# Kernel optimization log

Hardware: AMD Instinct MI355X
Metric: run time of the kernel (lower is better)

The kernel has to match this reference:

```python
import jax, jax.numpy as jnp
import numpy as np

B, T, H, NH, V = 2, 2048, 512, 8, 32000
HD = H // NH  # head dim

def setup_inputs() -> dict:
    key = jax.random.key(0)
    ks = jax.random.split(key, 15)
    s = 0.02
    rn = lambda k, shp: (jax.random.normal(k, shp, dtype=jnp.float32) * s)
    return {
        "ixs": jax.random.randint(ks[0], (B, T), 0, V, dtype=jnp.int32),
        "tok_emb": rn(ks[1], (V, H)),
        "pos_emb": rn(ks[2], (1, T, H)),
        "W_prj": rn(ks[3], (H, H)),
        "Wq": rn(ks[4], (H, H)), "bq": rn(ks[5], (H,)),
        "Wk": rn(ks[6], (H, H)), "bk": rn(ks[7], (H,)),
        "Wv": rn(ks[8], (H, H)), "bv": rn(ks[9], (H,)),
        "W1": rn(ks[10], (H, H)), "b1": rn(ks[11], (H,)),
        "W2": rn(ks[12], (V, H)), "b2": rn(ks[13], (V,)),
    }

def reference(ixs, tok_emb, pos_emb, W_prj, Wq, bq, Wk, bk, Wv, bv, W1, b1, W2, b2):
    b, t = ixs.shape
    # embeddings + projection (prj1 has no bias)
    x = tok_emb[ixs] + pos_emb[:, :t, :]          # [B,T,H]
    x = x @ W_prj.T                                # [B,T,H]
    # multi-head causal attention; NOTE: scale uses full hidden dim (allH**0.5)
    def heads(W, bias):
        return (x @ W.T + bias).reshape(b, t, NH, HD).transpose(0, 2, 1, 3)  # [B,nH,T,HD]
    q, k, v = heads(Wq, bq), heads(Wk, bk), heads(Wv, bv)
    att = jnp.einsum('bhqd,bhkd->bhqk', q, k) / (H ** 0.5)  # [B,nH,T,T]
    causal = jnp.tril(jnp.ones((t, t), dtype=bool))
    att = jnp.where(causal, att, -jnp.inf)
    w = jax.nn.softmax(att, axis=-1)
    y = jnp.einsum('bhqk,bhkd->bhqd', w, v)        # [B,nH,T,HD]
    y = y.transpose(0, 2, 1, 3).reshape(b, t, H)   # [B,T,H]
    # MLP: Linear->ReLU->Linear->ReLU (final ReLU per original loop condition)
    h1 = jax.nn.relu(y @ W1.T + b1)                # [B,T,H]
    out = jax.nn.relu(h1 @ W2.T + b2)              # [B,T,V]
    return out
```

## Files before the change

### kernel.cpp

```cpp
#include <hip/hip_runtime.h>
#include <stdint.h>
#include <stddef.h>

#define TSEQ   2048
#define HDIM   512
#define NHEADS 8
#define HEADD  64
#define NVOCAB 32000
#define NROWS  4096

typedef unsigned short ushort_t;
typedef __bf16 bf16x8 __attribute__((ext_vector_type(8)));
typedef float  f32x4  __attribute__((ext_vector_type(4)));
typedef unsigned short us8 __attribute__((ext_vector_type(8)));
typedef unsigned short us4 __attribute__((ext_vector_type(4)));
typedef unsigned short us2 __attribute__((ext_vector_type(2)));

__device__ __forceinline__ ushort_t f2bf(float f){
  union { float f; unsigned int u; } v; v.f = f;
  unsigned int u = v.u;
  u += 0x7FFFu + ((u >> 16) & 1u);
  return (ushort_t)(u >> 16);
}

__device__ __forceinline__ void gload_lds16(const ushort_t* g, ushort_t* l){
  __builtin_amdgcn_global_load_lds(
      (const __attribute__((address_space(1))) void*)g,
      (__attribute__((address_space(3))) void*)l, 16, 0, 0);
}

#define CVT_N4   4423680
#define CVT_TOT  4424064
__global__ void cvt_all_kernel(const float* __restrict__ Wprj, const float* __restrict__ Wq,
                               const float* __restrict__ Wk,   const float* __restrict__ Wv,
                               const float* __restrict__ W1,   const float* __restrict__ W2,
                               const float* __restrict__ bq,   const float* __restrict__ bk,
                               const float* __restrict__ bv,
                               ushort_t* __restrict__ wdst, float* __restrict__ bqkv){
  int stride = gridDim.x * blockDim.x;
  for (int i = blockIdx.x * blockDim.x + threadIdx.x; i < CVT_TOT; i += stride){
    if (i < CVT_N4){
      const float* src; int j;
      if (i < 327680){
        int w = i >> 16;
        j = i & 65535;
        src = (w == 0) ? Wprj : (w == 1) ? Wq : (w == 2) ? Wk : (w == 3) ? Wv : W1;
      } else {
        j = i - 327680;
        src = W2;
      }
      float4 f = ((const float4*)src)[j];
      us4 o;
      o[0] = f2bf(f.x); o[1] = f2bf(f.y); o[2] = f2bf(f.z); o[3] = f2bf(f.w);
      ((us4*)wdst)[i] = o;
    } else {
      int j = i - CVT_N4;
      const float* src = (j < 128) ? bq : (j < 256) ? bk : bv;
      int jj = j & 127;
      ((float4*)bqkv)[j] = ((const float4*)src)[jj];
    }
  }
}

__global__ void embed_kernel(const int* __restrict__ ixs, const float* __restrict__ tok,
                             const float* __restrict__ pos, ushort_t* __restrict__ x0){
  const int r = blockIdx.x;
  const int t = r & (TSEQ - 1);
  const int ix = ixs[r];
  const int j = threadIdx.x;
  const float2 a = ((const float2*)(tok + (size_t)ix * HDIM))[j];
  const float2 p = ((const float2*)(pos + (size_t)t * HDIM))[j];
  us2 o; o[0] = f2bf(a.x + p.x); o[1] = f2bf(a.y + p.y);
  *(us2*)(x0 + (size_t)r * HDIM + j * 2) = o;
}

template<int HAS_BIAS, int RELU, int OUT_F32>
__global__ __launch_bounds__(256) void gemm_bt_kernel(
    const ushort_t* __restrict__ A, const ushort_t* __restrict__ W,
    const float* __restrict__ bias, void* __restrict__ outp,
    int M, int N, int K)
{
  __shared__ ushort_t As[128 * 64];
  __shared__ ushort_t Bs[128 * 64];
  const int tid  = threadIdx.x;
  const int wave = tid >> 6;
  const int lane = tid & 63;
  const int lr   = lane & 15;
  const int lg   = lane >> 4;
  const int nby  = M >> 7;
  const int by   = blockIdx.x % nby;
  const int bx   = blockIdx.x / nby;
  const int row0 = by << 7;
  const int col0 = bx << 7;
  const int wr   = wave >> 1, wc = wave & 1;

  f32x4 acc[4][4];
#pragma unroll
  for (int m = 0; m < 4; m++)
#pragma unroll
    for (int n = 0; n < 4; n++) acc[m][n] = (f32x4){0.f, 0.f, 0.f, 0.f};

  const int e    = tid * 8;
  const int srow = e >> 6;
  const int scol = e & 63;
  const ushort_t* gA = A + (size_t)(row0 + srow) * K + scol;
  const ushort_t* gB = W + (size_t)(col0 + srow) * K + scol;
  const int ldsbase = wave * 512;

  for (int kt = 0; kt < K; kt += 64){
#pragma unroll
    for (int p = 0; p < 4; p++){
      gload_lds16(gA + (size_t)(p * 32) * K + kt, &As[p * 2048 + ldsbase]);
      gload_lds16(gB + (size_t)(p * 32) * K + kt, &Bs[p * 2048 + ldsbase]);
    }
    __syncthreads();
#pragma unroll
    for (int kk = 0; kk < 64; kk += 32){
      bf16x8 af[4], bfr[4];
#pragma unroll
      for (int m = 0; m < 4; m++)
        af[m] = __builtin_bit_cast(bf16x8,
            *(const us8*)&As[(wr * 64 + m * 16 + lr) * 64 + kk + lg * 8]);
#pragma unroll
      for (int n = 0; n < 4; n++)
        bfr[n] = __builtin_bit_cast(bf16x8,
            *(const us8*)&Bs[(wc * 64 + n * 16 + lr) * 64 + kk + lg * 8]);
#pragma unroll
      for (int m = 0; m < 4; m++)
#pragma unroll
        for (int n = 0; n < 4; n++)
          acc[m][n] = __builtin_amdgcn_mfma_f32_16x16x32_bf16(af[m], bfr[n], acc[m][n], 0, 0, 0);
    }
    __syncthreads();
  }

#pragma unroll
  for (int n = 0; n < 4; n++){
    const int col = col0 + wc * 64 + n * 16 + lr;
    float bv = 0.f;
    if (HAS_BIAS) bv = bias[col];
#pragma unroll
    for (int m = 0; m < 4; m++){
      const int rowb = row0 + wr * 64 + m * 16 + lg * 4;
#pragma unroll
      for (int r = 0; r < 4; r++){
        float vv = acc[m][n][r] + bv;
        if (RELU) vv = fmaxf(vv, 0.f);
        const size_t o = (size_t)(rowb + r) * N + col;
        if (OUT_F32) ((float*)outp)[o] = vv;
        else         ((ushort_t*)outp)[o] = f2bf(vv);
      }
    }
  }
}

__global__ __launch_bounds__(256) void attn_kernel(
    const ushort_t* __restrict__ qkv, ushort_t* __restrict__ y)
{
  __shared__ ushort_t Ks[64 * 64];
  __shared__ ushort_t Vt[64 * 64];
  __shared__ ushort_t Ps[4][16 * 64];
  const int qt   = blockIdx.x;
  const int hb   = blockIdx.y;
  const int b    = hb >> 3;
  const int h    = hb & 7;
  const int tid  = threadIdx.x;
  const int wave = tid >> 6, lane = tid & 63;
  const int lr   = lane & 15, lg = lane >> 4;
  const int ld   = 3 * HDIM;
  const size_t rowbase = (size_t)b * TSEQ;
  const ushort_t* kb = qkv + HDIM;
  const ushort_t* vb = qkv + 2 * HDIM;

  const int qrow = qt * 64 + wave * 16 + lr;
  const ushort_t* qp = qkv + (rowbase + qrow) * ld + h * HEADD;
  bf16x8 qf[2];
  qf[0] = __builtin_bit_cast(bf16x8, *(const us8*)&qp[lg * 8]);
  qf[1] = __builtin_bit_cast(bf16x8, *(const us8*)&qp[32 + lg * 8]);

  float m_run[4], l_run[4];
  f32x4 acc_o[4];
#pragma unroll
  for (int i = 0; i < 4; i++){ m_run[i] = -1e30f; l_run[i] = 0.f; acc_o[i] = (f32x4){0,0,0,0}; }

  const int e    = tid * 8;
  const int srow = e >> 6;
  const int scol = e & 63;
  const float scale = 0.04419417382415922f;

  for (int kt = 0; kt <= qt; ++kt){
    const ushort_t* gK = kb + (rowbase + kt * 64 + srow) * ld + h * HEADD + scol;
    gload_lds16(gK,                     &Ks[wave * 512]);
    gload_lds16(gK + (size_t)32 * ld,   &Ks[2048 + wave * 512]);
    const ushort_t* gV = vb + (rowbase + kt * 64 + srow) * ld + h * HEADD + scol;
    us8 v0 = *(const us8*)gV;
    us8 v1 = *(const us8*)(gV + (size_t)32 * ld);
#pragma unroll
    for (int j = 0; j < 8; j++){
      Vt[(scol + j) * 64 + srow]      = v0[j];
      Vt[(scol + j) * 64 + srow + 32] = v1[j];
    }
    __syncthreads();

    f32x4 s[4];
#pragma unroll
    for (int n = 0; n < 4; n++){
      s[n] = (f32x4){0, 0, 0, 0};
#pragma unroll
      for (int ks = 0; ks < 2; ks++){
        bf16x8 kf = __builtin_bit_cast(bf16x8,
            *(const us8*)&Ks[(n * 16 + lr) * 64 + ks * 32 + lg * 8]);
        s[n] = __builtin_amdgcn_mfma_f32_16x16x32_bf16(qf[ks], kf, s[n], 0, 0, 0);
      }
    }

    float sv[4][4];
    float tmax[4] = {-1e30f, -1e30f, -1e30f, -1e30f};
    const bool diag = (kt == qt);
#pragma unroll
    for (int n = 0; n < 4; n++)
#pragma unroll
      for (int r = 0; r < 4; r++){
        float x = s[n][r] * scale;
        if (diag && (n * 16 + lr) > (wave * 16 + lg * 4 + r)) x = -1e30f;
        sv[n][r] = x;
        tmax[r] = fmaxf(tmax[r], x);
      }
#pragma unroll
    for (int off = 1; off < 16; off <<= 1)
#pragma unroll
      for (int r = 0; r < 4; r++) tmax[r] = fmaxf(tmax[r], __shfl_xor(tmax[r], off));

    float alpha[4], psum[4];
#pragma unroll
    for (int r = 0; r < 4; r++){
      float mn = fmaxf(m_run[r], tmax[r]);
      alpha[r] = __expf(m_run[r] - mn);
      m_run[r] = mn;
      psum[r] = 0.f;
    }
    float p[4][4];
#pragma unroll
    for (int n = 0; n < 4; n++)
#pragma unroll
      for (int r = 0; r < 4; r++){ p[n][r] = __expf(sv[n][r] - m_run[r]); psum[r] += p[n][r]; }
#pragma unroll
    for (int off = 1; off < 16; off <<= 1)
#pragma unroll
      for (int r = 0; r < 4; r++) psum[r] += __shfl_xor(psum[r], off);
#pragma unroll
    for (int r = 0; r < 4; r++) l_run[r] = l_run[r] * alpha[r] + psum[r];
#pragma unroll
    for (int nd = 0; nd < 4; nd++)
#pragma unroll
      for (int r = 0; r < 4; r++) acc_o[nd][r] *= alpha[r];

#pragma unroll
    for (int n = 0; n < 4; n++)
#pragma unroll
      for (int r = 0; r < 4; r++)
        Ps[wave][(lg * 4 + r) * 64 + n * 16 + lr] = f2bf(p[n][r]);
    asm volatile("s_waitcnt lgkmcnt(0)" ::: "memory");
    bf16x8 pa[2];
    pa[0] = __builtin_bit_cast(bf16x8, *(const us8*)&Ps[wave][lr * 64 + lg * 8]);
    pa[1] = __builtin_bit_cast(bf16x8, *(const us8*)&Ps[wave][lr * 64 + 32 + lg * 8]);
#pragma unroll
    for (int nd = 0; nd < 4; nd++)
#pragma unroll
      for (int ks = 0; ks < 2; ks++){
        bf16x8 vf = __builtin_bit_cast(bf16x8,
            *(const us8*)&Vt[(nd * 16 + lr) * 64 + ks * 32 + lg * 8]);
        acc_o[nd] = __builtin_amdgcn_mfma_f32_16x16x32_bf16(pa[ks], vf, acc_o[nd], 0, 0, 0);
      }
    __syncthreads();
  }

  float inv[4];
#pragma unroll
  for (int r = 0; r < 4; r++) inv[r] = 1.f / l_run[r];
#pragma unroll
  for (int nd = 0; nd < 4; nd++)
#pragma unroll
    for (int r = 0; r < 4; r++){
      const int row_t = qt * 64 + wave * 16 + lg * 4 + r;
      y[(rowbase + row_t) * HDIM + h * HEADD + nd * 16 + lr] = f2bf(acc_o[nd][r] * inv[r]);
    }
}

extern "C" void kernel_launch(void* const* d_in, const int* in_sizes, int n_in,
                              void* d_out, int out_size, void* d_ws, size_t ws_size,
                              hipStream_t stream)
{
  const int*   ixs  = (const int*)  d_in[0];
  const float* tok  = (const float*)d_in[1];
  const float* pos  = (const float*)d_in[2];
  const float* Wprj = (const float*)d_in[3];
  const float* Wq   = (const float*)d_in[4];
  const float* bq_  = (const float*)d_in[5];
  const float* Wk   = (const float*)d_in[6];
  const float* bk_  = (const float*)d_in[7];
  const float* Wv   = (const float*)d_in[8];
  const float* bv_  = (const float*)d_in[9];
  const float* W1   = (const float*)d_in[10];
  const float* b1_  = (const float*)d_in[11];
  const float* W2   = (const float*)d_in[12];
  const float* b2_  = (const float*)d_in[13];
  float* out = (float*)d_out;

  ushort_t* ws    = (ushort_t*)d_ws;
  ushort_t* x0    = ws;
  ushort_t* x1    = x0    + 2097152;
  ushort_t* qkv   = x1    + 2097152;
  ushort_t* yb    = qkv   + 6291456;
  ushort_t* h1b   = yb    + 2097152;
  ushort_t* wprjb = h1b   + 2097152;
  ushort_t* wqkvb = wprjb + 262144;
  ushort_t* w1b   = wqkvb + 786432;
  ushort_t* w2b   = w1b   + 262144;
  float*    bqkv  = (float*)(w2b + 16384000);

  cvt_all_kernel<<<2048, 256, 0, stream>>>(Wprj, Wq, Wk, Wv, W1, W2,
                                           bq_, bk_, bv_, wprjb, bqkv);

  embed_kernel<<<NROWS, 256, 0, stream>>>(ixs, tok, pos, x0);

  gemm_bt_kernel<0,0,0><<<32 * 4,   256, 0, stream>>>(x0,  wprjb, nullptr, x1,  NROWS, 512,   512);
  gemm_bt_kernel<1,0,0><<<32 * 12,  256, 0, stream>>>(x1,  wqkvb, bqkv,    qkv, NROWS, 1536,  512);
  attn_kernel<<<dim3(32, 16), 256, 0, stream>>>(qkv, yb);
  gemm_bt_kernel<1,1,0><<<32 * 4,   256, 0, stream>>>(yb,  w1b,   b1_,     h1b, NROWS, 512,   512);
  gemm_bt_kernel<1,1,1><<<32 * 250, 256, 0, stream>>>(h1b, w2b,   b2_,     out, NROWS, NVOCAB, 512);
}
```

Baseline: 476.5 us.

## Add 256x256-tile triple-buffered GEMM kernel for vocab projection

```diff
diff --git a/kernel.cpp b/kernel.cpp
--- a/kernel.cpp
+++ b/kernel.cpp
@@ -154,6 +154,124 @@
   }
 }
 
+#define NKT 16
+__global__ __launch_bounds__(512, 2) void gemm_big_kernel(
+    const ushort_t* __restrict__ A, const ushort_t* __restrict__ W,
+    const float* __restrict__ bias, float* __restrict__ outp,
+    int M, int N, int K)
+{
+  __shared__ ushort_t Asb[3][256 * 32];
+  __shared__ ushort_t Bsb[3][256 * 32];
+  const int tid  = threadIdx.x;
+  const int wave = tid >> 6;
+  const int lane = tid & 63;
+  const int lr   = lane & 15;
+  const int lg   = lane >> 4;
+  const int wr   = wave >> 2;
+  const int wc   = wave & 3;
+  const int nby  = M >> 8;
+  const int by   = blockIdx.x % nby;
+  const int bx   = blockIdx.x / nby;
+  const int row0 = by << 8;
+  const int col0 = bx << 8;
+
+  const int rA   = tid >> 2;
+  const int csw  = ((tid & 3) ^ (rA & 3)) * 8;
+  const int swzc = (lg ^ (lr & 3)) * 8;
+
+  f32x4 acc[8][4];
+#pragma unroll
+  for (int m = 0; m < 8; m++)
+#pragma unroll
+    for (int n = 0; n < 4; n++) acc[m][n] = (f32x4){0.f, 0.f, 0.f, 0.f};
+
+  {
+    const ushort_t* gA = A + (size_t)(row0 + rA) * K + csw;
+    const ushort_t* gW = W + (size_t)(col0 + rA) * K + csw;
+#pragma unroll
+    for (int t = 0; t < 2; t++){
+      gload_lds16(gA + t * 32,                       &Asb[t][wave * 512]);
+      gload_lds16(gA + (size_t)128 * K + t * 32,     &Asb[t][4096 + wave * 512]);
+      gload_lds16(gW + t * 32,                       &Bsb[t][wave * 512]);
+      gload_lds16(gW + (size_t)128 * K + t * 32,     &Bsb[t][4096 + wave * 512]);
+    }
+  }
+  asm volatile("s_waitcnt vmcnt(4)" ::: "memory");
+  __builtin_amdgcn_s_barrier();
+
+  for (int t = 0; t < NKT; ++t){
+    const ushort_t* Ac = &Asb[t % 3][0];
+    const ushort_t* Bc = &Bsb[t % 3][0];
+    ushort_t* An = &Asb[(t + 2) % 3][0];
+    ushort_t* Bn = &Bsb[(t + 2) % 3][0];
+    const bool pf = (t + 2 < NKT);
+    const int kg = (t + 2) * 32;
+
+    bf16x8 bfr[4], af[4];
+#pragma unroll
+    for (int n = 0; n < 4; n++)
+      bfr[n] = __builtin_bit_cast(bf16x8,
+          *(const us8*)&Bc[(wc * 64 + n * 16 + lr) * 32 + swzc]);
+#pragma unroll
+    for (int q = 0; q < 4; q++)
+      af[q] = __builtin_bit_cast(bf16x8,
+          *(const us8*)&Ac[(wr * 128 + q * 16 + lr) * 32 + swzc]);
+    if (pf){
+      gload_lds16(A + (size_t)(row0 + rA) * K + kg + csw,       An + wave * 512);
+      gload_lds16(A + (size_t)(row0 + rA + 128) * K + kg + csw, An + 4096 + wave * 512);
+    }
+    __builtin_amdgcn_s_barrier();
+    asm volatile("s_waitcnt lgkmcnt(0)" ::: "memory");
+    __builtin_amdgcn_sched_barrier(0);
+    __builtin_amdgcn_s_setprio(1);
+#pragma unroll
+    for (int q = 0; q < 4; q++)
+#pragma unroll
+      for (int n = 0; n < 4; n++)
+        acc[q][n] = __builtin_amdgcn_mfma_f32_16x16x32_bf16(af[q], bfr[n], acc[q][n], 0, 0, 0);
+    __builtin_amdgcn_s_setprio(0);
+    __builtin_amdgcn_sched_barrier(0);
+    __builtin_amdgcn_s_barrier();
+
+#pragma unroll
+    for (int q = 0; q < 4; q++)
+      af[q] = __builtin_bit_cast(bf16x8,
+          *(const us8*)&Ac[(wr * 128 + (q + 4) * 16 + lr) * 32 + swzc]);
+    if (pf){
+      gload_lds16(W + (size_t)(col0 + rA) * K + kg + csw,       Bn + wave * 512);
+      gload_lds16(W + (size_t)(col0 + rA + 128) * K + kg + csw, Bn + 4096 + wave * 512);
+    }
+    __builtin_amdgcn_s_barrier();
+    asm volatile("s_waitcnt lgkmcnt(0)" ::: "memory");
+    __builtin_amdgcn_sched_barrier(0);
+    __builtin_amdgcn_s_setprio(1);
+#pragma unroll
+    for (int q = 0; q < 4; q++)
+#pragma unroll
+      for (int n = 0; n < 4; n++)
+        acc[q + 4][n] = __builtin_amdgcn_mfma_f32_16x16x32_bf16(af[q], bfr[n], acc[q + 4][n], 0, 0, 0);
+    __builtin_amdgcn_s_setprio(0);
+    __builtin_amdgcn_sched_barrier(0);
+    if (t < NKT - 2) { asm volatile("s_waitcnt vmcnt(4)" ::: "memory"); }
+    else             { asm volatile("s_waitcnt vmcnt(0)" ::: "memory"); }
+    __builtin_amdgcn_s_barrier();
+  }
+
+  float bvv[4];
+#pragma unroll
+  for (int n = 0; n < 4; n++) bvv[n] = bias[col0 + wc * 64 + n * 16 + lr];
+#pragma unroll
+  for (int m = 0; m < 8; m++)
+#pragma unroll
+    for (int n = 0; n < 4; n++){
+      const size_t o0 = (size_t)(row0 + wr * 128 + m * 16 + lg * 4) * N
+                      + (col0 + wc * 64 + n * 16 + lr);
+#pragma unroll
+      for (int r = 0; r < 4; r++)
+        outp[o0 + (size_t)r * N] = fmaxf(acc[m][n][r] + bvv[n], 0.f);
+    }
+}
+
 __global__ __launch_bounds__(256) void attn_kernel(
     const ushort_t* __restrict__ qkv, ushort_t* __restrict__ y)
 {
@@ -328,5 +446,5 @@
   gemm_bt_kernel<1,0,0><<<32 * 12,  256, 0, stream>>>(x1,  wqkvb, bqkv,    qkv, NROWS, 1536,  512);
   attn_kernel<<<dim3(32, 16), 256, 0, stream>>>(qkv, yb);
   gemm_bt_kernel<1,1,0><<<32 * 4,   256, 0, stream>>>(yb,  w1b,   b1_,     h1b, NROWS, 512,   512);
-  gemm_bt_kernel<1,1,1><<<32 * 250, 256, 0, stream>>>(h1b, w2b,   b2_,     out, NROWS, NVOCAB, 512);
-}
+  gemm_big_kernel<<<16 * 125, 512, 0, stream>>>(h1b, w2b, b2_, out, NROWS, NVOCAB, 512);
+}
```

Result: faster. 402.6 us (-15.5%).

## Double-buffer GEMM LDS tiles with swizzle, XCD block remap, reverse attention tile order

Applied to the files above, without the earlier changes.

```diff
diff --git a/kernel.cpp b/kernel.cpp
--- a/kernel.cpp
+++ b/kernel.cpp
@@ -75,24 +75,28 @@
 }
 
 template<int HAS_BIAS, int RELU, int OUT_F32>
-__global__ __launch_bounds__(256) void gemm_bt_kernel(
+__global__ __launch_bounds__(256) void gemm2_kernel(
     const ushort_t* __restrict__ A, const ushort_t* __restrict__ W,
     const float* __restrict__ bias, void* __restrict__ outp,
     int M, int N, int K)
 {
-  __shared__ ushort_t As[128 * 64];
-  __shared__ ushort_t Bs[128 * 64];
+  __shared__ ushort_t As[2][128 * 64];
+  __shared__ ushort_t Bs[2][128 * 64];
   const int tid  = threadIdx.x;
   const int wave = tid >> 6;
   const int lane = tid & 63;
   const int lr   = lane & 15;
   const int lg   = lane >> 4;
-  const int nby  = M >> 7;
-  const int by   = blockIdx.x % nby;
-  const int bx   = blockIdx.x / nby;
+  const int wr   = wave >> 1, wc = wave & 1;
+
+  const int nwg = gridDim.x;
+  const int cpx = nwg >> 3;
+  const int g   = (blockIdx.x & 7) * cpx + (blockIdx.x >> 3);
+  const int nby = M >> 7;
+  const int by  = g % nby;
+  const int bx  = g / nby;
   const int row0 = by << 7;
   const int col0 = bx << 7;
-  const int wr   = wave >> 1, wc = wave & 1;
 
   f32x4 acc[4][4];
 #pragma unroll
@@ -102,29 +106,41 @@
 
   const int e    = tid * 8;
   const int srow = e >> 6;
-  const int scol = e & 63;
-  const ushort_t* gA = A + (size_t)(row0 + srow) * K + scol;
-  const ushort_t* gB = W + (size_t)(col0 + srow) * K + scol;
-  const int ldsbase = wave * 512;
-
-  for (int kt = 0; kt < K; kt += 64){
-#pragma unroll
-    for (int p = 0; p < 4; p++){
-      gload_lds16(gA + (size_t)(p * 32) * K + kt, &As[p * 2048 + ldsbase]);
-      gload_lds16(gB + (size_t)(p * 32) * K + kt, &Bs[p * 2048 + ldsbase]);
-    }
-    __syncthreads();
+  const int gch  = (((e & 63) >> 3) ^ (srow & 7)) * 8;
+  const ushort_t* gA = A + (size_t)(row0 + srow) * K + gch;
+  const ushort_t* gB = W + (size_t)(col0 + srow) * K + gch;
+  const int ldsoff = wave * 512;
+
+#pragma unroll
+  for (int p = 0; p < 4; p++){
+    gload_lds16(gA + (size_t)(p * 32) * K, &As[0][p * 2048 + ldsoff]);
+    gload_lds16(gB + (size_t)(p * 32) * K, &Bs[0][p * 2048 + ldsoff]);
+  }
+  __syncthreads();
+
+  const int NT = K >> 6;
+  for (int t = 0; t < NT; ++t){
+    const int cur = t & 1;
+    if (t + 1 < NT){
+      const int ko = (t + 1) << 6;
+#pragma unroll
+      for (int p = 0; p < 4; p++){
+        gload_lds16(gA + (size_t)(p * 32) * K + ko, &As[cur ^ 1][p * 2048 + ldsoff]);
+        gload_lds16(gB + (size_t)(p * 32) * K + ko, &Bs[cur ^ 1][p * 2048 + ldsoff]);
+      }
+    }
 #pragma unroll
     for (int kk = 0; kk < 64; kk += 32){
+      const int rch = (((kk >> 3) + lg) ^ (lr & 7)) * 8;
       bf16x8 af[4], bfr[4];
 #pragma unroll
       for (int m = 0; m < 4; m++)
         af[m] = __builtin_bit_cast(bf16x8,
-            *(const us8*)&As[(wr * 64 + m * 16 + lr) * 64 + kk + lg * 8]);
+            *(const us8*)&As[cur][(wr * 64 + m * 16 + lr) * 64 + rch]);
 #pragma unroll
       for (int n = 0; n < 4; n++)
         bfr[n] = __builtin_bit_cast(bf16x8,
-            *(const us8*)&Bs[(wc * 64 + n * 16 + lr) * 64 + kk + lg * 8]);
+            *(const us8*)&Bs[cur][(wc * 64 + n * 16 + lr) * 64 + rch]);
 #pragma unroll
       for (int m = 0; m < 4; m++)
 #pragma unroll
@@ -160,7 +176,7 @@
   __shared__ ushort_t Ks[64 * 64];
   __shared__ ushort_t Vt[64 * 64];
   __shared__ ushort_t Ps[4][16 * 64];
-  const int qt   = blockIdx.x;
+  const int qt   = 31 - blockIdx.x;
   const int hb   = blockIdx.y;
   const int b    = hb >> 3;
   const int h    = hb & 7;
@@ -324,9 +340,9 @@
 
   embed_kernel<<<NROWS, 256, 0, stream>>>(ixs, tok, pos, x0);
 
-  gemm_bt_kernel<0,0,0><<<32 * 4,   256, 0, stream>>>(x0,  wprjb, nullptr, x1,  NROWS, 512,   512);
-  gemm_bt_kernel<1,0,0><<<32 * 12,  256, 0, stream>>>(x1,  wqkvb, bqkv,    qkv, NROWS, 1536,  512);
+  gemm2_kernel<0,0,0><<<32 * 4,   256, 0, stream>>>(x0,  wprjb, nullptr, x1,  NROWS, 512,   512);
+  gemm2_kernel<1,0,0><<<32 * 12,  256, 0, stream>>>(x1,  wqkvb, bqkv,    qkv, NROWS, 1536,  512);
   attn_kernel<<<dim3(32, 16), 256, 0, stream>>>(qkv, yb);
-  gemm_bt_kernel<1,1,0><<<32 * 4,   256, 0, stream>>>(yb,  w1b,   b1_,     h1b, NROWS, 512,   512);
-  gemm_bt_kernel<1,1,1><<<32 * 250, 256, 0, stream>>>(h1b, w2b,   b2_,     out, NROWS, NVOCAB, 512);
-}
+  gemm2_kernel<1,1,0><<<32 * 4,   256, 0, stream>>>(yb,  w1b,   b1_,     h1b, NROWS, 512,   512);
+  gemm2_kernel<1,1,1><<<32 * 250, 256, 0, stream>>>(h1b, w2b,   b2_,     out, NROWS, NVOCAB, 512);
+}
```

New measurement: 501.9 us. +5.3%, slower.
